# Kernel tuning notes

Measured on AMD Instinct MI355X. Metric: run time of the kernel, lower is better.

Reference implementation:

```python
import jax, jax.numpy as jnp
import numpy as np

H, KD, VD = 12, 64, 64  # num_heads, k_dim, v_dim
EPS = 1e-12

def _l2norm(x, axis):
    n = jnp.linalg.norm(x, axis=axis, keepdims=True)
    return x / jnp.maximum(n, EPS)

def setup_inputs() -> dict:
    key = jax.random.key(0)
    ks = jax.random.split(key, 6)
    d1, d2 = 768, 768
    return {
        "x1": jax.random.normal(ks[0], (2048, d1), jnp.float32),
        "x2": jax.random.normal(ks[1], (8192, d2), jnp.float32),
        "Wq": jax.random.normal(ks[2], (H * KD, d1), jnp.float32) * 0.03,
        "Wk": jax.random.normal(ks[3], (H * KD, d2), jnp.float32) * 0.03,
        "Wv": jax.random.normal(ks[4], (H * VD, d2), jnp.float32) * 0.03,
        "Wo": jax.random.normal(ks[5], (d1, H * VD), jnp.float32) * 0.03,
        "invt": 20,
    }

def reference(x1, x2, Wq, Wk, Wv, Wo, invt):
    B1 = x1.shape[0]
    B2 = x2.shape[0]
    # Linear (no bias): y = x @ W.T, then split heads
    q = (x1 @ Wq.T).reshape(B1, H, KD)  # [B1,H,KD]
    k = (x2 @ Wk.T).reshape(B2, H, KD)  # [B2,H,KD]
    v = (x2 @ Wv.T).reshape(B2, H, VD)  # [B2,H,VD]
    # per-head L2 normalization over feature dim (cosine attention)
    q = _l2norm(q, axis=-1)
    k = _l2norm(k, axis=-1)
    attn = jnp.einsum("bhd,nhd->hbn", q, k) * jnp.float32(invt)  # [H,B1,B2]
    attn = jax.nn.softmax(attn, axis=-1)
    out = jnp.einsum("hbn,nhd->bhd", attn, v).reshape(B1, H * VD)
    out = out @ Wo.T  # [B1, in_dim1]
    return _l2norm(out, axis=1)
```

## Files before the change

kernel.cpp:

```cpp
#include <hip/hip_runtime.h>
#include <hip/hip_bf16.h>
#include <math.h>

#define B1 2048
#define B2 8192
#define NH 12
#define DH 64
#define DMODEL 768

typedef __attribute__((ext_vector_type(8))) short short8;
typedef __attribute__((ext_vector_type(4))) float floatx4;
typedef __attribute__((ext_vector_type(8))) unsigned short ushort8;
typedef __attribute__((ext_vector_type(4))) unsigned short ushort4v;

static __device__ __forceinline__ unsigned short f2bf(float f) {
  __bf16 b = (__bf16)f;
  return __builtin_bit_cast(unsigned short, b);
}
static __device__ __forceinline__ float bf2f(unsigned short u) {
  return __builtin_bit_cast(float, ((unsigned)u) << 16);
}

static __device__ __forceinline__ void gload16(const unsigned short* g,
                                               unsigned short* l) {
  __builtin_amdgcn_global_load_lds(
      (const __attribute__((address_space(1))) void*)g,
      (__attribute__((address_space(3))) void*)l, 16, 0, 0);
}

__global__ __launch_bounds__(256) void prep_all(
    const float* __restrict__ x1, unsigned short* __restrict__ x1h,
    unsigned short* __restrict__ x1l, const float* __restrict__ x2,
    unsigned short* __restrict__ x2h, unsigned short* __restrict__ x2l,
    const float* __restrict__ Wq, unsigned short* __restrict__ Wqh,
    unsigned short* __restrict__ Wql, const float* __restrict__ Wk,
    unsigned short* __restrict__ Wkh, unsigned short* __restrict__ Wkl,
    const float* __restrict__ Wv, unsigned short* __restrict__ Wvh,
    const float* __restrict__ Wo, unsigned short* __restrict__ Woh) {
  const int bi = blockIdx.x;
  const float* src;
  unsigned short *hi, *lo = nullptr;
  int lb;
  if (bi < 1536) {
    src = x1; hi = x1h; lo = x1l; lb = bi;
  } else if (bi < 7680) {
    src = x2; hi = x2h; lo = x2l; lb = bi - 1536;
  } else if (bi < 8256) {
    src = Wq; hi = Wqh; lo = Wql; lb = bi - 7680;
  } else if (bi < 8832) {
    src = Wk; hi = Wkh; lo = Wkl; lb = bi - 8256;
  } else if (bi < 9408) {
    src = Wv; hi = Wvh; lb = bi - 8832;
  } else {
    src = Wo; hi = Woh; lb = bi - 9408;
  }
  const int i = (lb * 256 + threadIdx.x) * 4;
  const float4 v = *(const float4*)&src[i];
  ushort4v h = {f2bf(v.x), f2bf(v.y), f2bf(v.z), f2bf(v.w)};
  *(ushort4v*)&hi[i] = h;
  if (lo) {
    ushort4v l = {f2bf(v.x - bf2f(h[0])), f2bf(v.y - bf2f(h[1])),
                  f2bf(v.z - bf2f(h[2])), f2bf(v.w - bf2f(h[3]))};
    *(ushort4v*)&lo[i] = l;
  }
}

template <bool SPLIT, bool L2N, bool F32OUT>
static __device__ __forceinline__ void gemm_tile(
    const unsigned short* __restrict__ Ahg, const unsigned short* __restrict__ Alg,
    const unsigned short* __restrict__ Bhg, const unsigned short* __restrict__ Blg,
    void* __restrict__ Cv, int M, int N, int K, int m0, int n0,
    unsigned short* sAh, unsigned short* sBh, unsigned short* sAl,
    unsigned short* sBl) {
  const int tid = threadIdx.x;
  const int wave = tid >> 6;
  const int lane = tid & 63;
  const int wm = wave >> 1;
  const int wn = wave & 1;
  const int n15 = lane & 15;
  const int quad = lane >> 4;
  const int srow = lane >> 2;
  const int cpl = (lane & 3) ^ (srow >> 2);

  floatx4 acc[4][4];
#pragma unroll
  for (int i = 0; i < 4; ++i)
#pragma unroll
    for (int j = 0; j < 4; ++j) acc[i][j] = (floatx4){0.f, 0.f, 0.f, 0.f};

  for (int k0 = 0; k0 < K; k0 += 32) {
    __syncthreads();
#pragma unroll
    for (int jj = 0; jj < 2; ++jj) {
      const int j = wave * 2 + jj;
      const int row = j * 16 + srow;
      const size_t goffA = (size_t)(m0 + row) * K + k0 + cpl * 8;
      const size_t goffB = (size_t)(n0 + row) * K + k0 + cpl * 8;
      gload16(Ahg + goffA, &sAh[j * 512]);
      gload16(Bhg + goffB, &sBh[j * 512]);
      if constexpr (SPLIT) {
        gload16(Alg + goffA, &sAl[j * 512]);
        gload16(Blg + goffB, &sBl[j * 512]);
      }
    }
    __syncthreads();

    short8 afh[4], afl[4];
#pragma unroll
    for (int mt = 0; mt < 4; ++mt) {
      const int row = wm * 64 + mt * 16 + n15;
      const int off = row * 32 + ((quad ^ (n15 >> 2)) << 3);
      afh[mt] = *(const short8*)&sAh[off];
      if constexpr (SPLIT) afl[mt] = *(const short8*)&sAl[off];
    }
#pragma unroll
    for (int nt = 0; nt < 4; ++nt) {
      const int row = wn * 64 + nt * 16 + n15;
      const int off = row * 32 + ((quad ^ (n15 >> 2)) << 3);
      const short8 bfh = *(const short8*)&sBh[off];
      if constexpr (SPLIT) {
        const short8 bfl = *(const short8*)&sBl[off];
#pragma unroll
        for (int mt = 0; mt < 4; ++mt) {
          acc[mt][nt] = __builtin_amdgcn_mfma_f32_16x16x32_bf16(afh[mt], bfh, acc[mt][nt], 0, 0, 0);
          acc[mt][nt] = __builtin_amdgcn_mfma_f32_16x16x32_bf16(afh[mt], bfl, acc[mt][nt], 0, 0, 0);
          acc[mt][nt] = __builtin_amdgcn_mfma_f32_16x16x32_bf16(afl[mt], bfh, acc[mt][nt], 0, 0, 0);
        }
      } else {
#pragma unroll
        for (int mt = 0; mt < 4; ++mt)
          acc[mt][nt] = __builtin_amdgcn_mfma_f32_16x16x32_bf16(afh[mt], bfh, acc[mt][nt], 0, 0, 0);
      }
    }
  }

#pragma unroll
  for (int mt = 0; mt < 4; ++mt) {
    float scalev[4] = {1.f, 1.f, 1.f, 1.f};
    if constexpr (L2N) {
#pragma unroll
      for (int rr = 0; rr < 4; ++rr) {
        float ss = 0.f;
#pragma unroll
        for (int nt = 0; nt < 4; ++nt) ss += acc[mt][nt][rr] * acc[mt][nt][rr];
        ss += __shfl_xor(ss, 1, 64);
        ss += __shfl_xor(ss, 2, 64);
        ss += __shfl_xor(ss, 4, 64);
        ss += __shfl_xor(ss, 8, 64);
        scalev[rr] = 1.0f / fmaxf(sqrtf(ss), 1e-12f);
      }
    }
#pragma unroll
    for (int nt = 0; nt < 4; ++nt) {
#pragma unroll
      for (int rr = 0; rr < 4; ++rr) {
        const int row = m0 + wm * 64 + mt * 16 + quad * 4 + rr;
        const int col = n0 + wn * 64 + nt * 16 + n15;
        const float v = acc[mt][nt][rr] * scalev[rr];
        if constexpr (F32OUT)
          ((float*)Cv)[(size_t)row * N + col] = v;
        else
          ((unsigned short*)Cv)[(size_t)row * N + col] = f2bf(v);
      }
    }
  }
}

__global__ __launch_bounds__(256) void qk_proj(
    const unsigned short* __restrict__ x1h, const unsigned short* __restrict__ x1l,
    const unsigned short* __restrict__ Wqh, const unsigned short* __restrict__ Wql,
    const unsigned short* __restrict__ x2h, const unsigned short* __restrict__ x2l,
    const unsigned short* __restrict__ Wkh, const unsigned short* __restrict__ Wkl,
    unsigned short* __restrict__ qbf, unsigned short* __restrict__ kbf) {
  __shared__ __align__(16) unsigned short sAh[4096], sBh[4096], sAl[4096], sBl[4096];
  const int bi = blockIdx.x;
  if (bi < 96) {
    gemm_tile<true, true, false>(x1h, x1l, Wqh, Wql, qbf, B1, DMODEL, DMODEL,
                                 (bi / 6) * 128, (bi % 6) * 128, sAh, sBh, sAl, sBl);
  } else {
    const int b = bi - 96;
    gemm_tile<true, true, false>(x2h, x2l, Wkh, Wkl, kbf, B2, DMODEL, DMODEL,
                                 (b / 6) * 128, (b % 6) * 128, sAh, sBh, sAl, sBl);
  }
}

__global__ __launch_bounds__(256) void v_zero(
    const unsigned short* __restrict__ Wvh, const unsigned short* __restrict__ x2h,
    unsigned short* __restrict__ vtbf, float* __restrict__ aoacc,
    float* __restrict__ lacc) {
  __shared__ __align__(16) unsigned short sAh[4096], sBh[4096];
  const int bi = blockIdx.x;
  if (bi < 384) {
    gemm_tile<false, false, false>(Wvh, nullptr, x2h, nullptr, vtbf, DMODEL, B2,
                                   DMODEL, (bi / 64) * 128, (bi % 64) * 128,
                                   sAh, sBh, nullptr, nullptr);
  } else if (bi < 768) {
    const float4 z = {0.f, 0.f, 0.f, 0.f};
    float4* p = (float4*)aoacc + (size_t)(bi - 384) * 1024 + threadIdx.x;
    p[0] = z; p[256] = z; p[512] = z; p[768] = z;
  } else {
    const float4 z = {0.f, 0.f, 0.f, 0.f};
    float4* p = (float4*)lacc + (size_t)(bi - 768) * 1024 + threadIdx.x;
    p[0] = z; p[256] = z; p[512] = z; p[768] = z;
  }
}

#define KC 128
#define KSPLIT 2
#define NCH (B2 / KSPLIT / KC)
#define PSTR 68

__global__ __launch_bounds__(256, 3) void attn_mfma(
    const unsigned short* __restrict__ qb, const unsigned short* __restrict__ kb,
    const unsigned short* __restrict__ vt, float* __restrict__ aoacc,
    float* __restrict__ lacc, const int* __restrict__ invt_p) {
  __shared__ __align__(16) unsigned short smem[25088];
  unsigned short* Kl = smem;
  unsigned short* Vl = smem + 8192;
  unsigned short* Psl = smem + 16384;

  const float c2 = (float)invt_p[0] * 1.4426950408889634f;
  const int h = blockIdx.y;
  const int q0 = blockIdx.x * 64;
  const int tid = threadIdx.x;
  const int wave = tid >> 6;
  const int lane = tid & 63;
  const int qsub = wave >> 1;
  const int ksub = wave & 1;
  const int n15 = lane & 15;
  const int quad = lane >> 4;
  const int kz0 = blockIdx.z * (B2 / KSPLIT);

  unsigned short* Ps = &Psl[wave * 32 * PSTR];

  short8 qf[2][2];
#pragma unroll
  for (int qt = 0; qt < 2; ++qt)
#pragma unroll
    for (int ks = 0; ks < 2; ++ks) {
      const int qrow = q0 + qsub * 32 + qt * 16 + n15;
      qf[qt][ks] = *(const short8*)&qb[(size_t)qrow * DMODEL + h * DH + ks * 32 + quad * 8];
    }

  floatx4 oacc[2][4];
#pragma unroll
  for (int qt = 0; qt < 2; ++qt)
#pragma unroll
    for (int nt = 0; nt < 4; ++nt) oacc[qt][nt] = (floatx4){0.f, 0.f, 0.f, 0.f};
  float lsum[2] = {0.f, 0.f};

  ushort8 kr[4], vr[4];
#pragma unroll
  for (int i = 0; i < 4; ++i) {
    const int s = i * 256 + tid;
    const int key = s >> 3, cpk = s & 7, chk = cpk ^ (key & 7);
    kr[i] = *(const ushort8*)&kb[(size_t)(kz0 + key) * DMODEL + h * DH + chk * 8];
    const int d = s >> 4, cpv = s & 15, chv = cpv ^ (d & 15);
    vr[i] = *(const ushort8*)&vt[(size_t)(h * DH + d) * B2 + kz0 + chv * 8];
  }

  for (int c = 0; c < NCH; ++c) {
    __syncthreads();
#pragma unroll
    for (int i = 0; i < 4; ++i) {
      const int s = i * 256 + tid;
      const int key = s >> 3, cpk = s & 7;
      *(ushort8*)&Kl[key * 64 + cpk * 8] = kr[i];
      const int d = s >> 4, cpv = s & 15;
      *(ushort8*)&Vl[d * 128 + cpv * 8] = vr[i];
    }
    if (c + 1 < NCH) {
      const int kc0n = kz0 + (c + 1) * KC;
#pragma unroll
      for (int i = 0; i < 4; ++i) {
        const int s = i * 256 + tid;
        const int key = s >> 3, cpk = s & 7, chk = cpk ^ (key & 7);
        kr[i] = *(const ushort8*)&kb[(size_t)(kc0n + key) * DMODEL + h * DH + chk * 8];
        const int d = s >> 4, cpv = s & 15, chv = cpv ^ (d & 15);
        vr[i] = *(const ushort8*)&vt[(size_t)(h * DH + d) * B2 + kc0n + chv * 8];
      }
    }
    __syncthreads();

#pragma unroll
    for (int kt = 0; kt < 4; ++kt) {
      floatx4 s0 = {0.f, 0.f, 0.f, 0.f}, s1 = {0.f, 0.f, 0.f, 0.f};
#pragma unroll
      for (int ks = 0; ks < 2; ++ks) {
        const int key = ksub * 64 + kt * 16 + n15;
        const int cp = (ks * 4 + quad) ^ (n15 & 7);
        const short8 kf = *(const short8*)&Kl[key * 64 + cp * 8];
        s0 = __builtin_amdgcn_mfma_f32_16x16x32_bf16(kf, qf[0][ks], s0, 0, 0, 0);
        s1 = __builtin_amdgcn_mfma_f32_16x16x32_bf16(kf, qf[1][ks], s1, 0, 0, 0);
      }
      ushort4v p0, p1;
#pragma unroll
      for (int r = 0; r < 4; ++r) {
        const float e0 = exp2f(fmaf(s0[r], c2, -c2));
        const float e1 = exp2f(fmaf(s1[r], c2, -c2));
        lsum[0] += e0;
        lsum[1] += e1;
        p0[r] = f2bf(e0);
        p1[r] = f2bf(e1);
      }
      *(ushort4v*)&Ps[(0 * 16 + n15) * PSTR + kt * 16 + quad * 4] = p0;
      *(ushort4v*)&Ps[(1 * 16 + n15) * PSTR + kt * 16 + quad * 4] = p1;
    }

#pragma unroll
    for (int ks = 0; ks < 2; ++ks) {
      short8 pa[2];
#pragma unroll
      for (int qt = 0; qt < 2; ++qt)
        pa[qt] = *(const short8*)&Ps[(qt * 16 + n15) * PSTR + ks * 32 + quad * 8];
#pragma unroll
      for (int nt = 0; nt < 4; ++nt) {
        const int dd = nt * 16 + n15;
        const int cp = (ksub * 8 + ks * 4 + quad) ^ (n15 & 15);
        const short8 vf = *(const short8*)&Vl[dd * 128 + cp * 8];
        oacc[0][nt] = __builtin_amdgcn_mfma_f32_16x16x32_bf16(pa[0], vf, oacc[0][nt], 0, 0, 0);
        oacc[1][nt] = __builtin_amdgcn_mfma_f32_16x16x32_bf16(pa[1], vf, oacc[1][nt], 0, 0, 0);
      }
    }
  }

#pragma unroll
  for (int qt = 0; qt < 2; ++qt) {
    float v = lsum[qt];
    v += __shfl_xor(v, 16, 64);
    v += __shfl_xor(v, 32, 64);
    lsum[qt] = v;
  }
  if (quad == 0) {
#pragma unroll
    for (int qt = 0; qt < 2; ++qt)
      atomicAdd(&lacc[(q0 + qsub * 32 + qt * 16 + n15) * NH + h], lsum[qt]);
  }

  __syncthreads();
  float* Osc = (float*)smem;
  if (ksub == 1) {
#pragma unroll
    for (int qt = 0; qt < 2; ++qt)
#pragma unroll
      for (int nt = 0; nt < 4; ++nt)
#pragma unroll
        for (int r = 0; r < 4; ++r) {
          const int row = qsub * 32 + qt * 16 + quad * 4 + r;
          Osc[row * 64 + nt * 16 + n15] = oacc[qt][nt][r];
        }
  }
  __syncthreads();
  if (ksub == 0) {
#pragma unroll
    for (int qt = 0; qt < 2; ++qt)
#pragma unroll
      for (int nt = 0; nt < 4; ++nt)
#pragma unroll
        for (int r = 0; r < 4; ++r) {
          const int row = qsub * 32 + qt * 16 + quad * 4 + r;
          const float v = oacc[qt][nt][r] + Osc[row * 64 + nt * 16 + n15];
          atomicAdd(&aoacc[(size_t)(q0 + row) * DMODEL + h * DH + nt * 16 + n15], v);
        }
  }
}

__global__ __launch_bounds__(256) void wo_proj(
    const float* __restrict__ aoacc, const float* __restrict__ lacc,
    const unsigned short* __restrict__ Woh, float* __restrict__ woout) {
  __shared__ __align__(16) unsigned short sAh[4096], sBh[4096];
  const int bi = blockIdx.x;
  const int m0 = (bi / 6) * 128;
  const int n0 = (bi % 6) * 128;
  const int tid = threadIdx.x;
  const int wave = tid >> 6;
  const int lane = tid & 63;
  const int wm = wave >> 1;
  const int wn = wave & 1;
  const int n15 = lane & 15;
  const int quad = lane >> 4;
  const int srow = lane >> 2;
  const int cpl = (lane & 3) ^ (srow >> 2);

  floatx4 acc[4][4];
#pragma unroll
  for (int i = 0; i < 4; ++i)
#pragma unroll
    for (int j = 0; j < 4; ++j) acc[i][j] = (floatx4){0.f, 0.f, 0.f, 0.f};

  for (int k0 = 0; k0 < DMODEL; k0 += 32) {
    __syncthreads();
#pragma unroll
    for (int jj = 0; jj < 2; ++jj) {
      const int j = wave * 2 + jj;
      const int row = j * 16 + srow;
      const size_t ga = (size_t)(m0 + row) * DMODEL + k0 + cpl * 8;
      const float4 a0 = *(const float4*)&aoacc[ga];
      const float4 a1 = *(const float4*)&aoacc[ga + 4];
      const int head = (k0 + cpl * 8) >> 6;
      const float inv = 1.0f / lacc[(m0 + row) * NH + head];
      ushort8 ah = {f2bf(a0.x * inv), f2bf(a0.y * inv), f2bf(a0.z * inv),
                    f2bf(a0.w * inv), f2bf(a1.x * inv), f2bf(a1.y * inv),
                    f2bf(a1.z * inv), f2bf(a1.w * inv)};
      *(ushort8*)&sAh[j * 512 + lane * 8] = ah;
      gload16(Woh + (size_t)(n0 + row) * DMODEL + k0 + cpl * 8, &sBh[j * 512]);
    }
    __syncthreads();

    short8 afh[4];
#pragma unroll
    for (int mt = 0; mt < 4; ++mt) {
      const int row = wm * 64 + mt * 16 + n15;
      afh[mt] = *(const short8*)&sAh[row * 32 + ((quad ^ (n15 >> 2)) << 3)];
    }
#pragma unroll
    for (int nt = 0; nt < 4; ++nt) {
      const int row = wn * 64 + nt * 16 + n15;
      const short8 bfh = *(const short8*)&sBh[row * 32 + ((quad ^ (n15 >> 2)) << 3)];
#pragma unroll
      for (int mt = 0; mt < 4; ++mt)
        acc[mt][nt] = __builtin_amdgcn_mfma_f32_16x16x32_bf16(afh[mt], bfh, acc[mt][nt], 0, 0, 0);
    }
  }

#pragma unroll
  for (int mt = 0; mt < 4; ++mt)
#pragma unroll
    for (int nt = 0; nt < 4; ++nt)
#pragma unroll
      for (int rr = 0; rr < 4; ++rr) {
        const int row = m0 + wm * 64 + mt * 16 + quad * 4 + rr;
        const int col = n0 + wn * 64 + nt * 16 + n15;
        woout[(size_t)row * DMODEL + col] = acc[mt][nt][rr];
      }
}

__global__ __launch_bounds__(256) void l2norm_rows768_out(
    const float* __restrict__ x, float* __restrict__ out) {
  const int row = blockIdx.x;
  const float* xr = &x[(size_t)row * DMODEL];
  float ss = 0.0f;
  float vals[3];
#pragma unroll
  for (int i = 0; i < 3; ++i) {
    vals[i] = xr[threadIdx.x + i * 256];
    ss += vals[i] * vals[i];
  }
#pragma unroll
  for (int off = 32; off > 0; off >>= 1) ss += __shfl_xor(ss, off, 64);
  __shared__ float ws[4];
  if ((threadIdx.x & 63) == 0) ws[threadIdx.x >> 6] = ss;
  __syncthreads();
  const float tot = ws[0] + ws[1] + ws[2] + ws[3];
  const float sc = 1.0f / fmaxf(sqrtf(tot), 1e-12f);
  float* orow = &out[(size_t)row * DMODEL];
#pragma unroll
  for (int i = 0; i < 3; ++i) orow[threadIdx.x + i * 256] = vals[i] * sc;
}

extern "C" void kernel_launch(void* const* d_in, const int* in_sizes, int n_in,
                              void* d_out, int out_size, void* d_ws,
                              size_t ws_size, hipStream_t stream) {
  const float* x1 = (const float*)d_in[0];
  const float* x2 = (const float*)d_in[1];
  const float* Wq = (const float*)d_in[2];
  const float* Wk = (const float*)d_in[3];
  const float* Wv = (const float*)d_in[4];
  const float* Wo = (const float*)d_in[5];
  const int* invt = (const int*)d_in[6];
  float* outp = (float*)d_out;

  char* ws = (char*)d_ws;
  unsigned short* x1h = (unsigned short*)(ws + 0);
  unsigned short* x1l = (unsigned short*)(ws + 3145728);
  unsigned short* x2h = (unsigned short*)(ws + 6291456);
  unsigned short* x2l = (unsigned short*)(ws + 18874368);
  unsigned short* Wqh = (unsigned short*)(ws + 31457280);
  unsigned short* Wql = (unsigned short*)(ws + 32636928);
  unsigned short* Wkh = (unsigned short*)(ws + 33816576);
  unsigned short* Wkl = (unsigned short*)(ws + 34996224);
  unsigned short* Wvh = (unsigned short*)(ws + 36175872);
  unsigned short* Woh = (unsigned short*)(ws + 37355520);
  unsigned short* q_bf = (unsigned short*)(ws + 38535168);
  unsigned short* k_bf = (unsigned short*)(ws + 41680896);
  float* lacc = (float*)(ws + 54263808);
  float* aoacc = (float*)(ws + 0);
  unsigned short* vt_bf = (unsigned short*)(ws + 18874368);
  float* woout = (float*)(ws + 9437184);

  prep_all<<<9984, 256, 0, stream>>>(x1, x1h, x1l, x2, x2h, x2l, Wq, Wqh, Wql,
                                     Wk, Wkh, Wkl, Wv, Wvh, Wo, Woh);
  qk_proj<<<480, 256, 0, stream>>>(x1h, x1l, Wqh, Wql, x2h, x2l, Wkh, Wkl,
                                   q_bf, k_bf);
  v_zero<<<774, 256, 0, stream>>>(Wvh, x2h, vt_bf, aoacc, lacc);
  attn_mfma<<<dim3(B1 / 64, NH, KSPLIT), 256, 0, stream>>>(q_bf, k_bf, vt_bf,
                                                           aoacc, lacc, invt);
  wo_proj<<<96, 256, 0, stream>>>(aoacc, lacc, Woh, woout);
  l2norm_rows768_out<<<B1, 256, 0, stream>>>(woout, outp);
}
```

Measured before the change: 308.3 us.

## Switch attention to 32x32x16 MFMA with register-resident P via cross-lane shuffles

Rewrites the attention inner loop to use 32x32x16 bf16 MFMAs instead of 16x16x32. The exponentiated score tile is repacked in registers with xor-32 lane shuffles to form the A operand of the PV product, which removes the LDS round-trip for P and shrinks shared memory. The key split is raised from 2 to 4 and occupancy from 3 to 4 blocks per CU to expose more parallelism. The cost is twice as many atomic adds into the output and row-sum accumulators, plus more shuffle traffic.

After: 373.6 us. 21.2% more time.

```diff
diff --git a/kernel.cpp b/kernel.cpp
--- a/kernel.cpp
+++ b/kernel.cpp
@@ -10,8 +10,10 @@
 
 typedef __attribute__((ext_vector_type(8))) short short8;
 typedef __attribute__((ext_vector_type(4))) float floatx4;
+typedef __attribute__((ext_vector_type(16))) float floatx16;
 typedef __attribute__((ext_vector_type(8))) unsigned short ushort8;
 typedef __attribute__((ext_vector_type(4))) unsigned short ushort4v;
+typedef __attribute__((ext_vector_type(4))) unsigned int uintx4;
 
 static __device__ __forceinline__ unsigned short f2bf(float f) {
   __bf16 b = (__bf16)f;
@@ -206,18 +208,16 @@
 }
 
 #define KC 128
-#define KSPLIT 2
+#define KSPLIT 4
 #define NCH (B2 / KSPLIT / KC)
-#define PSTR 68
-
-__global__ __launch_bounds__(256, 3) void attn_mfma(
+
+__global__ __launch_bounds__(256, 4) void attn_mfma(
     const unsigned short* __restrict__ qb, const unsigned short* __restrict__ kb,
     const unsigned short* __restrict__ vt, float* __restrict__ aoacc,
     float* __restrict__ lacc, const int* __restrict__ invt_p) {
-  __shared__ __align__(16) unsigned short smem[25088];
+  __shared__ __align__(16) unsigned short smem[16384];
   unsigned short* Kl = smem;
   unsigned short* Vl = smem + 8192;
-  unsigned short* Psl = smem + 16384;
 
   const float c2 = (float)invt_p[0] * 1.4426950408889634f;
   const int h = blockIdx.y;
@@ -227,27 +227,24 @@
   const int lane = tid & 63;
   const int qsub = wave >> 1;
   const int ksub = wave & 1;
-  const int n15 = lane & 15;
-  const int quad = lane >> 4;
+  const int l31 = lane & 31;
+  const int hi = lane >> 5;
   const int kz0 = blockIdx.z * (B2 / KSPLIT);
 
-  unsigned short* Ps = &Psl[wave * 32 * PSTR];
-
-  short8 qf[2][2];
-#pragma unroll
-  for (int qt = 0; qt < 2; ++qt)
-#pragma unroll
-    for (int ks = 0; ks < 2; ++ks) {
-      const int qrow = q0 + qsub * 32 + qt * 16 + n15;
-      qf[qt][ks] = *(const short8*)&qb[(size_t)qrow * DMODEL + h * DH + ks * 32 + quad * 8];
-    }
-
-  floatx4 oacc[2][4];
-#pragma unroll
-  for (int qt = 0; qt < 2; ++qt)
-#pragma unroll
-    for (int nt = 0; nt < 4; ++nt) oacc[qt][nt] = (floatx4){0.f, 0.f, 0.f, 0.f};
-  float lsum[2] = {0.f, 0.f};
+  short8 qf[4];
+  {
+    const int qrow = q0 + qsub * 32 + l31;
+#pragma unroll
+    for (int m = 0; m < 4; ++m)
+      qf[m] = *(const short8*)&qb[(size_t)qrow * DMODEL + h * DH + m * 16 + hi * 8];
+  }
+
+  floatx16 oacc[2];
+#pragma unroll
+  for (int dt = 0; dt < 2; ++dt)
+#pragma unroll
+    for (int r = 0; r < 16; ++r) oacc[dt][r] = 0.f;
+  float lsum = 0.f;
 
   ushort8 kr[4], vr[4];
 #pragma unroll
@@ -283,85 +280,78 @@
     __syncthreads();
 
 #pragma unroll
-    for (int kt = 0; kt < 4; ++kt) {
-      floatx4 s0 = {0.f, 0.f, 0.f, 0.f}, s1 = {0.f, 0.f, 0.f, 0.f};
-#pragma unroll
-      for (int ks = 0; ks < 2; ++ks) {
-        const int key = ksub * 64 + kt * 16 + n15;
-        const int cp = (ks * 4 + quad) ^ (n15 & 7);
-        const short8 kf = *(const short8*)&Kl[key * 64 + cp * 8];
-        s0 = __builtin_amdgcn_mfma_f32_16x16x32_bf16(kf, qf[0][ks], s0, 0, 0, 0);
-        s1 = __builtin_amdgcn_mfma_f32_16x16x32_bf16(kf, qf[1][ks], s1, 0, 0, 0);
-      }
-      ushort4v p0, p1;
-#pragma unroll
-      for (int r = 0; r < 4; ++r) {
-        const float e0 = exp2f(fmaf(s0[r], c2, -c2));
-        const float e1 = exp2f(fmaf(s1[r], c2, -c2));
-        lsum[0] += e0;
-        lsum[1] += e1;
-        p0[r] = f2bf(e0);
-        p1[r] = f2bf(e1);
-      }
-      *(ushort4v*)&Ps[(0 * 16 + n15) * PSTR + kt * 16 + quad * 4] = p0;
-      *(ushort4v*)&Ps[(1 * 16 + n15) * PSTR + kt * 16 + quad * 4] = p1;
-    }
-
-#pragma unroll
-    for (int ks = 0; ks < 2; ++ks) {
-      short8 pa[2];
-#pragma unroll
-      for (int qt = 0; qt < 2; ++qt)
-        pa[qt] = *(const short8*)&Ps[(qt * 16 + n15) * PSTR + ks * 32 + quad * 8];
-#pragma unroll
-      for (int nt = 0; nt < 4; ++nt) {
-        const int dd = nt * 16 + n15;
-        const int cp = (ksub * 8 + ks * 4 + quad) ^ (n15 & 15);
-        const short8 vf = *(const short8*)&Vl[dd * 128 + cp * 8];
-        oacc[0][nt] = __builtin_amdgcn_mfma_f32_16x16x32_bf16(pa[0], vf, oacc[0][nt], 0, 0, 0);
-        oacc[1][nt] = __builtin_amdgcn_mfma_f32_16x16x32_bf16(pa[1], vf, oacc[1][nt], 0, 0, 0);
-      }
-    }
-  }
-
-#pragma unroll
-  for (int qt = 0; qt < 2; ++qt) {
-    float v = lsum[qt];
-    v += __shfl_xor(v, 16, 64);
-    v += __shfl_xor(v, 32, 64);
-    lsum[qt] = v;
-  }
-  if (quad == 0) {
-#pragma unroll
-    for (int qt = 0; qt < 2; ++qt)
-      atomicAdd(&lacc[(q0 + qsub * 32 + qt * 16 + n15) * NH + h], lsum[qt]);
-  }
+    for (int kt = 0; kt < 2; ++kt) {
+      floatx16 s;
+#pragma unroll
+      for (int r = 0; r < 16; ++r) s[r] = 0.f;
+      const int keyrow = ksub * 64 + kt * 32 + l31;
+#pragma unroll
+      for (int m = 0; m < 4; ++m) {
+        const int g = (2 * m + hi) ^ (keyrow & 7);
+        const short8 kf = *(const short8*)&Kl[keyrow * 64 + g * 8];
+        s = __builtin_amdgcn_mfma_f32_32x32x16_bf16(kf, qf[m], s, 0, 0, 0);
+      }
+      unsigned pk[8];
+#pragma unroll
+      for (int i = 0; i < 8; ++i) {
+        const float e0 = exp2f(fmaf(s[2 * i], c2, -c2));
+        const float e1 = exp2f(fmaf(s[2 * i + 1], c2, -c2));
+        lsum += e0 + e1;
+        pk[i] = (unsigned)f2bf(e0) | ((unsigned)f2bf(e1) << 16);
+      }
+      const unsigned sel02 = hi ? pk[0] : pk[2];
+      const unsigned sel13 = hi ? pk[1] : pk[3];
+      const unsigned sel46 = hi ? pk[4] : pk[6];
+      const unsigned sel57 = hi ? pk[5] : pk[7];
+      const unsigned x02 = (unsigned)__shfl_xor((int)sel02, 32, 64);
+      const unsigned x13 = (unsigned)__shfl_xor((int)sel13, 32, 64);
+      const unsigned x46 = (unsigned)__shfl_xor((int)sel46, 32, 64);
+      const unsigned x57 = (unsigned)__shfl_xor((int)sel57, 32, 64);
+      const uintx4 w0 = {hi ? x02 : pk[0], hi ? x13 : pk[1],
+                         hi ? pk[2] : x02, hi ? pk[3] : x13};
+      const uintx4 w1 = {hi ? x46 : pk[4], hi ? x57 : pk[5],
+                         hi ? pk[6] : x46, hi ? pk[7] : x57};
+      const short8 pa0 = __builtin_bit_cast(short8, w0);
+      const short8 pa1 = __builtin_bit_cast(short8, w1);
+#pragma unroll
+      for (int dt = 0; dt < 2; ++dt) {
+        const int d = dt * 32 + l31;
+        const int swz = l31 & 15;
+        const short8 vf0 =
+            *(const short8*)&Vl[d * 128 + ((ksub * 8 + kt * 4 + hi) ^ swz) * 8];
+        const short8 vf1 =
+            *(const short8*)&Vl[d * 128 + ((ksub * 8 + kt * 4 + 2 + hi) ^ swz) * 8];
+        oacc[dt] = __builtin_amdgcn_mfma_f32_32x32x16_bf16(pa0, vf0, oacc[dt], 0, 0, 0);
+        oacc[dt] = __builtin_amdgcn_mfma_f32_32x32x16_bf16(pa1, vf1, oacc[dt], 0, 0, 0);
+      }
+    }
+  }
+
+  lsum += __shfl_xor(lsum, 32, 64);
+  if (hi == 0)
+    atomicAdd(&lacc[(q0 + qsub * 32 + l31) * NH + h], lsum);
 
   __syncthreads();
   float* Osc = (float*)smem;
   if (ksub == 1) {
 #pragma unroll
-    for (int qt = 0; qt < 2; ++qt)
-#pragma unroll
-      for (int nt = 0; nt < 4; ++nt)
-#pragma unroll
-        for (int r = 0; r < 4; ++r) {
-          const int row = qsub * 32 + qt * 16 + quad * 4 + r;
-          Osc[row * 64 + nt * 16 + n15] = oacc[qt][nt][r];
-        }
+    for (int dt = 0; dt < 2; ++dt)
+#pragma unroll
+      for (int r = 0; r < 16; ++r) {
+        const int row = qsub * 32 + (r & 3) + 8 * (r >> 2) + 4 * hi;
+        Osc[row * 64 + dt * 32 + l31] = oacc[dt][r];
+      }
   }
   __syncthreads();
   if (ksub == 0) {
 #pragma unroll
-    for (int qt = 0; qt < 2; ++qt)
-#pragma unroll
-      for (int nt = 0; nt < 4; ++nt)
-#pragma unroll
-        for (int r = 0; r < 4; ++r) {
-          const int row = qsub * 32 + qt * 16 + quad * 4 + r;
-          const float v = oacc[qt][nt][r] + Osc[row * 64 + nt * 16 + n15];
-          atomicAdd(&aoacc[(size_t)(q0 + row) * DMODEL + h * DH + nt * 16 + n15], v);
-        }
+    for (int dt = 0; dt < 2; ++dt)
+#pragma unroll
+      for (int r = 0; r < 16; ++r) {
+        const int row = qsub * 32 + (r & 3) + 8 * (r >> 2) + 4 * hi;
+        const float v = oacc[dt][r] + Osc[row * 64 + dt * 32 + l31];
+        atomicAdd(&aoacc[(size_t)(q0 + row) * DMODEL + h * DH + dt * 32 + l31], v);
+      }
   }
 }
 
```

## Read K/V directly from global in attention and replace atomics with split-K partial buffers

Applied to the files above, without the earlier changes.

The attention kernel stops staging K and V chunks through LDS with register prefetch and reads MFMA fragments straight from global memory, which shrinks shared memory per block and removes per-chunk barriers. Separately, the split-K halves now write their output and row-sum partials to separate buffers instead of using atomicAdd. wo_proj sums the two partials, so the zeroing work in the V-projection kernel is dropped. Direct global reads give up LDS reuse and swizzled access, so K/V loads become strided, with more cache traffic and possible latency stalls.

After: 373.8 us. 21.3% more time.

```diff
diff --git a/kernel.cpp b/kernel.cpp
--- a/kernel.cpp
+++ b/kernel.cpp
@@ -184,25 +184,14 @@
   }
 }
 
-__global__ __launch_bounds__(256) void v_zero(
+__global__ __launch_bounds__(256) void v_proj(
     const unsigned short* __restrict__ Wvh, const unsigned short* __restrict__ x2h,
-    unsigned short* __restrict__ vtbf, float* __restrict__ aoacc,
-    float* __restrict__ lacc) {
+    unsigned short* __restrict__ vtbf) {
   __shared__ __align__(16) unsigned short sAh[4096], sBh[4096];
   const int bi = blockIdx.x;
-  if (bi < 384) {
-    gemm_tile<false, false, false>(Wvh, nullptr, x2h, nullptr, vtbf, DMODEL, B2,
-                                   DMODEL, (bi / 64) * 128, (bi % 64) * 128,
-                                   sAh, sBh, nullptr, nullptr);
-  } else if (bi < 768) {
-    const float4 z = {0.f, 0.f, 0.f, 0.f};
-    float4* p = (float4*)aoacc + (size_t)(bi - 384) * 1024 + threadIdx.x;
-    p[0] = z; p[256] = z; p[512] = z; p[768] = z;
-  } else {
-    const float4 z = {0.f, 0.f, 0.f, 0.f};
-    float4* p = (float4*)lacc + (size_t)(bi - 768) * 1024 + threadIdx.x;
-    p[0] = z; p[256] = z; p[512] = z; p[768] = z;
-  }
+  gemm_tile<false, false, false>(Wvh, nullptr, x2h, nullptr, vtbf, DMODEL, B2,
+                                 DMODEL, (bi / 64) * 128, (bi % 64) * 128,
+                                 sAh, sBh, nullptr, nullptr);
 }
 
 #define KC 128
@@ -214,10 +203,7 @@
     const unsigned short* __restrict__ qb, const unsigned short* __restrict__ kb,
     const unsigned short* __restrict__ vt, float* __restrict__ aoacc,
     float* __restrict__ lacc, const int* __restrict__ invt_p) {
-  __shared__ __align__(16) unsigned short smem[25088];
-  unsigned short* Kl = smem;
-  unsigned short* Vl = smem + 8192;
-  unsigned short* Psl = smem + 16384;
+  __shared__ __align__(16) unsigned short smem[8704];
 
   const float c2 = (float)invt_p[0] * 1.4426950408889634f;
   const int h = blockIdx.y;
@@ -231,7 +217,7 @@
   const int quad = lane >> 4;
   const int kz0 = blockIdx.z * (B2 / KSPLIT);
 
-  unsigned short* Ps = &Psl[wave * 32 * PSTR];
+  unsigned short* Ps = &smem[wave * 32 * PSTR];
 
   short8 qf[2][2];
 #pragma unroll
@@ -249,47 +235,20 @@
     for (int nt = 0; nt < 4; ++nt) oacc[qt][nt] = (floatx4){0.f, 0.f, 0.f, 0.f};
   float lsum[2] = {0.f, 0.f};
 
-  ushort8 kr[4], vr[4];
-#pragma unroll
-  for (int i = 0; i < 4; ++i) {
-    const int s = i * 256 + tid;
-    const int key = s >> 3, cpk = s & 7, chk = cpk ^ (key & 7);
-    kr[i] = *(const ushort8*)&kb[(size_t)(kz0 + key) * DMODEL + h * DH + chk * 8];
-    const int d = s >> 4, cpv = s & 15, chv = cpv ^ (d & 15);
-    vr[i] = *(const ushort8*)&vt[(size_t)(h * DH + d) * B2 + kz0 + chv * 8];
-  }
+  const unsigned short* kbp = kb + (size_t)kz0 * DMODEL + h * DH;
+  const unsigned short* vbp = vt + (size_t)(h * DH) * B2 + kz0;
 
   for (int c = 0; c < NCH; ++c) {
-    __syncthreads();
-#pragma unroll
-    for (int i = 0; i < 4; ++i) {
-      const int s = i * 256 + tid;
-      const int key = s >> 3, cpk = s & 7;
-      *(ushort8*)&Kl[key * 64 + cpk * 8] = kr[i];
-      const int d = s >> 4, cpv = s & 15;
-      *(ushort8*)&Vl[d * 128 + cpv * 8] = vr[i];
-    }
-    if (c + 1 < NCH) {
-      const int kc0n = kz0 + (c + 1) * KC;
-#pragma unroll
-      for (int i = 0; i < 4; ++i) {
-        const int s = i * 256 + tid;
-        const int key = s >> 3, cpk = s & 7, chk = cpk ^ (key & 7);
-        kr[i] = *(const ushort8*)&kb[(size_t)(kc0n + key) * DMODEL + h * DH + chk * 8];
-        const int d = s >> 4, cpv = s & 15, chv = cpv ^ (d & 15);
-        vr[i] = *(const ushort8*)&vt[(size_t)(h * DH + d) * B2 + kc0n + chv * 8];
-      }
-    }
-    __syncthreads();
+    const unsigned short* kc_ = kbp + (size_t)c * KC * DMODEL;
+    const unsigned short* vc_ = vbp + c * KC;
 
 #pragma unroll
     for (int kt = 0; kt < 4; ++kt) {
       floatx4 s0 = {0.f, 0.f, 0.f, 0.f}, s1 = {0.f, 0.f, 0.f, 0.f};
 #pragma unroll
       for (int ks = 0; ks < 2; ++ks) {
-        const int key = ksub * 64 + kt * 16 + n15;
-        const int cp = (ks * 4 + quad) ^ (n15 & 7);
-        const short8 kf = *(const short8*)&Kl[key * 64 + cp * 8];
+        const short8 kf = *(const short8*)&kc_[
+            (size_t)(ksub * 64 + kt * 16 + n15) * DMODEL + (ks * 4 + quad) * 8];
         s0 = __builtin_amdgcn_mfma_f32_16x16x32_bf16(kf, qf[0][ks], s0, 0, 0, 0);
         s1 = __builtin_amdgcn_mfma_f32_16x16x32_bf16(kf, qf[1][ks], s1, 0, 0, 0);
       }
@@ -315,9 +274,8 @@
         pa[qt] = *(const short8*)&Ps[(qt * 16 + n15) * PSTR + ks * 32 + quad * 8];
 #pragma unroll
       for (int nt = 0; nt < 4; ++nt) {
-        const int dd = nt * 16 + n15;
-        const int cp = (ksub * 8 + ks * 4 + quad) ^ (n15 & 15);
-        const short8 vf = *(const short8*)&Vl[dd * 128 + cp * 8];
+        const short8 vf = *(const short8*)&vc_[
+            (size_t)(nt * 16 + n15) * B2 + (ksub * 8 + ks * 4 + quad) * 8];
         oacc[0][nt] = __builtin_amdgcn_mfma_f32_16x16x32_bf16(pa[0], vf, oacc[0][nt], 0, 0, 0);
         oacc[1][nt] = __builtin_amdgcn_mfma_f32_16x16x32_bf16(pa[1], vf, oacc[1][nt], 0, 0, 0);
       }
@@ -331,14 +289,13 @@
     v += __shfl_xor(v, 32, 64);
     lsum[qt] = v;
   }
-  if (quad == 0) {
-#pragma unroll
-    for (int qt = 0; qt < 2; ++qt)
-      atomicAdd(&lacc[(q0 + qsub * 32 + qt * 16 + n15) * NH + h], lsum[qt]);
-  }
+
+  float* aoz = aoacc + (size_t)blockIdx.z * B1 * DMODEL;
+  float* lz = lacc + (size_t)blockIdx.z * B1 * NH;
 
   __syncthreads();
   float* Osc = (float*)smem;
+  float* lsc = Osc + 4096;
   if (ksub == 1) {
 #pragma unroll
     for (int qt = 0; qt < 2; ++qt)
@@ -349,6 +306,10 @@
           const int row = qsub * 32 + qt * 16 + quad * 4 + r;
           Osc[row * 64 + nt * 16 + n15] = oacc[qt][nt][r];
         }
+    if (quad == 0) {
+      lsc[qsub * 32 + n15] = lsum[0];
+      lsc[qsub * 32 + 16 + n15] = lsum[1];
+    }
   }
   __syncthreads();
   if (ksub == 0) {
@@ -360,8 +321,13 @@
         for (int r = 0; r < 4; ++r) {
           const int row = qsub * 32 + qt * 16 + quad * 4 + r;
           const float v = oacc[qt][nt][r] + Osc[row * 64 + nt * 16 + n15];
-          atomicAdd(&aoacc[(size_t)(q0 + row) * DMODEL + h * DH + nt * 16 + n15], v);
+          aoz[(size_t)(q0 + row) * DMODEL + h * DH + nt * 16 + n15] = v;
         }
+    if (quad == 0) {
+      lz[(size_t)(q0 + qsub * 32 + n15) * NH + h] = lsum[0] + lsc[qsub * 32 + n15];
+      lz[(size_t)(q0 + qsub * 32 + 16 + n15) * NH + h] =
+          lsum[1] + lsc[qsub * 32 + 16 + n15];
+    }
   }
 }
 
@@ -382,6 +348,9 @@
   const int srow = lane >> 2;
   const int cpl = (lane & 3) ^ (srow >> 2);
 
+  const float* ao1 = aoacc + (size_t)B1 * DMODEL;
+  const float* la1 = lacc + (size_t)B1 * NH;
+
   floatx4 acc[4][4];
 #pragma unroll
   for (int i = 0; i < 4; ++i)
@@ -397,11 +366,15 @@
       const size_t ga = (size_t)(m0 + row) * DMODEL + k0 + cpl * 8;
       const float4 a0 = *(const float4*)&aoacc[ga];
       const float4 a1 = *(const float4*)&aoacc[ga + 4];
+      const float4 b0 = *(const float4*)&ao1[ga];
+      const float4 b1 = *(const float4*)&ao1[ga + 4];
       const int head = (k0 + cpl * 8) >> 6;
-      const float inv = 1.0f / lacc[(m0 + row) * NH + head];
-      ushort8 ah = {f2bf(a0.x * inv), f2bf(a0.y * inv), f2bf(a0.z * inv),
-                    f2bf(a0.w * inv), f2bf(a1.x * inv), f2bf(a1.y * inv),
-                    f2bf(a1.z * inv), f2bf(a1.w * inv)};
+      const float lsum = lacc[(m0 + row) * NH + head] + la1[(m0 + row) * NH + head];
+      const float inv = 1.0f / lsum;
+      ushort8 ah = {f2bf((a0.x + b0.x) * inv), f2bf((a0.y + b0.y) * inv),
+                    f2bf((a0.z + b0.z) * inv), f2bf((a0.w + b0.w) * inv),
+                    f2bf((a1.x + b1.x) * inv), f2bf((a1.y + b1.y) * inv),
+                    f2bf((a1.z + b1.z) * inv), f2bf((a1.w + b1.w) * inv)};
       *(ushort8*)&sAh[j * 512 + lane * 8] = ah;
       gload16(Woh + (size_t)(n0 + row) * DMODEL + k0 + cpl * 8, &sBh[j * 512]);
     }
@@ -483,16 +456,16 @@
   unsigned short* Woh = (unsigned short*)(ws + 37355520);
   unsigned short* q_bf = (unsigned short*)(ws + 38535168);
   unsigned short* k_bf = (unsigned short*)(ws + 41680896);
-  float* lacc = (float*)(ws + 54263808);
   float* aoacc = (float*)(ws + 0);
+  float* lacc = (float*)(ws + 32636928);
   unsigned short* vt_bf = (unsigned short*)(ws + 18874368);
-  float* woout = (float*)(ws + 9437184);
+  float* woout = (float*)(ws + 12582912);
 
   prep_all<<<9984, 256, 0, stream>>>(x1, x1h, x1l, x2, x2h, x2l, Wq, Wqh, Wql,
                                      Wk, Wkh, Wkl, Wv, Wvh, Wo, Woh);
   qk_proj<<<480, 256, 0, stream>>>(x1h, x1l, Wqh, Wql, x2h, x2l, Wkh, Wkl,
                                    q_bf, k_bf);
-  v_zero<<<774, 256, 0, stream>>>(Wvh, x2h, vt_bf, aoacc, lacc);
+  v_proj<<<384, 256, 0, stream>>>(Wvh, x2h, vt_bf);
   attn_mfma<<<dim3(B1 / 64, NH, KSPLIT), 256, 0, stream>>>(q_bf, k_bf, vt_bf,
                                                            aoacc, lacc, invt);
   wo_proj<<<96, 256, 0, stream>>>(aoacc, lacc, Woh, woout);
```
